# Kernel tuning notes

Measured on AMD Instinct MI355X. Metric: run time of the kernel, lower is better.

The kernel has to match this reference:

```python
import jax, jax.numpy as jnp
import numpy as np

D = 768

def setup_inputs() -> dict:
    key = jax.random.key(0)
    ks = jax.random.split(key, 12)
    inp = {
        "text_embeddings": jax.random.normal(ks[0], (8, 512, D), dtype=jnp.float32),
        "kb_emb": jax.random.normal(ks[1], (200000, D), dtype=jnp.float32),
        "W_ret": jax.random.normal(ks[2], (D, D), dtype=jnp.float32) * 0.02,
        "b_ret": jax.random.normal(ks[3], (D,), dtype=jnp.float32) * 0.02,
        "Ws1": jax.random.normal(ks[4], (2 * D, D), dtype=jnp.float32) * 0.02,
        "bs1": jax.random.normal(ks[5], (D,), dtype=jnp.float32) * 0.02,
        "Ws2": jax.random.normal(ks[6], (D, 1), dtype=jnp.float32) * 0.02,
        "bs2": jax.random.normal(ks[7], (1,), dtype=jnp.float32) * 0.02,
        "mention_sent": jax.random.randint(ks[8], (256,), 0, 8, dtype=jnp.int32),
        "mention_start": jax.random.randint(ks[9], (256,), 0, 480, dtype=jnp.int32),
        "mention_len": jax.random.randint(ks[10], (256,), 0, 31, dtype=jnp.int32),
        "top_k": 100,
    }
    return inp


def reference(text_embeddings, kb_emb, W_ret, b_ret, Ws1, bs1, Ws2, bs2,
              mention_sent, mention_start, mention_len, top_k):
    S = text_embeddings.shape[1]
    pos = jnp.arange(S, dtype=jnp.int32)
    # inclusive span [start, start+len] -> mask [M, S]
    mask = (pos[None, :] >= mention_start[:, None]) & (pos[None, :] <= (mention_start + mention_len)[:, None])
    maskf = mask.astype(text_embeddings.dtype)
    sent = text_embeddings[mention_sent]                       # [M, S, D]
    mention_emb = jnp.einsum('msd,ms->md', sent, maskf) / maskf.sum(1, keepdims=True)

    # entity_retriever linear, then KB dot-product retrieval of top 2k candidates
    query = mention_emb @ W_ret.T + b_ret                      # [M, D]
    sims = query @ kb_emb.T                                    # [M, N]
    _, cand_idx = jax.lax.top_k(sims, 2 * top_k)               # [M, 2k]
    cand_embs = kb_emb[cand_idx]                               # [M, 2k, D]

    # candidate_scorer: Linear(2D->D) on concat(mention, cand) + ReLU + Linear(D->1) + Sigmoid
    m_part = mention_emb @ Ws1[:D]                             # [M, D]
    c_part = jnp.einsum('mkd,de->mke', cand_embs, Ws1[D:])     # [M, 2k, D]
    h = jax.nn.relu(m_part[:, None, :] + c_part + bs1)
    scores = jax.nn.sigmoid(jnp.einsum('mke,eo->mko', h, Ws2)[..., 0] + bs2[0])  # [M, 2k]

    top_scores, ti = jax.lax.top_k(scores, top_k)              # [M, k]
    top_kb_idx = jnp.take_along_axis(cand_idx, ti, axis=1)
    return top_scores, top_kb_idx
```

## Files before the change

kernel.cpp:

```cpp
#include <hip/hip_runtime.h>
#include <cfloat>
#include <cmath>
#include <cstdint>

#define DD 768
#define MM 256
#define NKB 200000
#define SLEN 512
#define KK 200
#define TOPK 100
#define SURV_CAP 1024
#define RESC 232
#define THRC 2.70f
#define MAXMARK 32768
#define DELTA 4e-5
#define NET 12

typedef __attribute__((ext_vector_type(8))) short bf16x8;
typedef __attribute__((ext_vector_type(4))) float f32x4;

__device__ __forceinline__ unsigned short f2bf_rne(float x) {
  unsigned u = __float_as_uint(x);
  unsigned r = (u + 0x7FFFu + ((u >> 16) & 1u)) >> 16;
  return (unsigned short)r;
}
__device__ __forceinline__ float bf2f(unsigned short us) {
  return __uint_as_float(((unsigned)us) << 16);
}
__device__ __forceinline__ void splitbf(float x, unsigned short& hi, unsigned short& lo) {
  hi = f2bf_rne(x);
  lo = f2bf_rne(x - bf2f(hi));
}

__global__ __launch_bounds__(256) void k_mention_emb(
    const float* __restrict__ text, const int* __restrict__ msent,
    const int* __restrict__ mstart, const int* __restrict__ mlen,
    double* __restrict__ me64) {
  int m = blockIdx.x;
  int sent = msent[m], st = mstart[m], ln = mlen[m];
  const float* base = text + (size_t)sent * SLEN * DD;
  for (int d = threadIdx.x; d < DD; d += blockDim.x) {
    double acc = 0.0;
    for (int s = st; s <= st + ln; ++s) acc += (double)base[(size_t)s * DD + d];
    me64[(size_t)m * DD + d] = acc / (double)(ln + 1);
  }
}

__global__ __launch_bounds__(256) void k_query(
    const double* __restrict__ me64, const float* __restrict__ Wret,
    const float* __restrict__ bret, double* __restrict__ q64,
    unsigned short* __restrict__ qb16, float* __restrict__ tthr) {
  int m = blockIdx.x;
  __shared__ double sme[DD];
  __shared__ float snorm[256];
  for (int d = threadIdx.x; d < DD; d += blockDim.x) sme[d] = me64[(size_t)m * DD + d];
  __syncthreads();
  float nloc = 0.f;
  for (int e = threadIdx.x; e < DD; e += blockDim.x) {
    double acc = (double)bret[e];
    const float* wr = Wret + (size_t)e * DD;
    for (int d = 0; d < DD; ++d) acc += sme[d] * (double)wr[d];
    q64[(size_t)m * DD + e] = acc;
    qb16[(size_t)m * DD + e] = f2bf_rne((float)acc);
    nloc += (float)(acc * acc);
  }
  snorm[threadIdx.x] = nloc; __syncthreads();
  for (int s = 128; s > 0; s >>= 1) {
    if (threadIdx.x < s) snorm[threadIdx.x] += snorm[threadIdx.x + s];
    __syncthreads();
  }
  if (threadIdx.x == 0) tthr[m] = THRC * sqrtf(snorm[0]);
}

__global__ __launch_bounds__(256) void k_mpart(
    const double* __restrict__ me64, const float* __restrict__ Ws1,
    double* __restrict__ mp64, float* __restrict__ mp32) {
  int m = blockIdx.x;
  __shared__ double sme[DD];
  for (int d = threadIdx.x; d < DD; d += blockDim.x) sme[d] = me64[(size_t)m * DD + d];
  __syncthreads();
  for (int e = threadIdx.x; e < DD; e += blockDim.x) {
    double acc = 0.0;
    for (int d = 0; d < DD; ++d) acc += sme[d] * (double)Ws1[(size_t)d * DD + e];
    mp64[(size_t)m * DD + e] = acc;
    mp32[(size_t)m * DD + e] = (float)acc;
  }
}

__global__ __launch_bounds__(256) void k_prep(
    const float* __restrict__ Ws1, unsigned short* __restrict__ Bth,
    unsigned short* __restrict__ Btl) {
  int e = blockIdx.x;
  for (int k = threadIdx.x; k < DD; k += 256) {
    float x = Ws1[(size_t)(DD + k) * DD + e];
    unsigned short hi, lo;
    splitbf(x, hi, lo);
    Bth[(size_t)e * DD + k] = hi;
    Btl[(size_t)e * DD + k] = lo;
  }
}

__global__ __launch_bounds__(256) void k_sims_mfma(
    const unsigned short* __restrict__ qb, const float* __restrict__ kb,
    const float* __restrict__ tthr, int* __restrict__ gcnt,
    uint2* __restrict__ gcand) {
  __shared__ unsigned short As[256 * 32];
  __shared__ unsigned short Bs[64 * 32];
  __shared__ float sthr[256];
  int n0 = blockIdx.x * 64;
  int tid = threadIdx.x;
  int lane = tid & 63, w = tid >> 6;
  int h = lane >> 4, c = lane & 15;
  sthr[tid] = tthr[tid];
  f32x4 acc[4][4] = {};
  for (int k0 = 0; k0 < DD; k0 += 32) {
#pragma unroll
    for (int i = 0; i < 4; ++i) {
      int idx = tid + i * 256;
      int m = idx >> 2, q4 = idx & 3;
      uint4 v = *(const uint4*)(qb + (size_t)m * DD + k0 + q4 * 8);
      int off = (m * 64 + q4 * 16) ^ ((m & 7) << 4);
      *(uint4*)((char*)As + off) = v;
    }
#pragma unroll
    for (int i = 0; i < 2; ++i) {
      int idx = tid + i * 256;
      int n = idx >> 3, f4 = idx & 7;
      float4 v = *(const float4*)(kb + (size_t)(n0 + n) * DD + k0 + f4 * 4);
      uint2 p;
      p.x = (unsigned)f2bf_rne(v.x) | ((unsigned)f2bf_rne(v.y) << 16);
      p.y = (unsigned)f2bf_rne(v.z) | ((unsigned)f2bf_rne(v.w) << 16);
      int off = (n * 64 + f4 * 8) ^ ((n & 7) << 4);
      *(uint2*)((char*)Bs + off) = p;
    }
    __syncthreads();
    bf16x8 a[4], b[4];
#pragma unroll
    for (int mf = 0; mf < 4; ++mf) {
      int m = w * 64 + mf * 16 + c;
      int off = (m * 64 + h * 16) ^ ((m & 7) << 4);
      a[mf] = *(bf16x8*)((char*)As + off);
    }
#pragma unroll
    for (int nf = 0; nf < 4; ++nf) {
      int n = nf * 16 + c;
      int off = (n * 64 + h * 16) ^ ((n & 7) << 4);
      b[nf] = *(bf16x8*)((char*)Bs + off);
    }
#pragma unroll
    for (int mf = 0; mf < 4; ++mf)
#pragma unroll
      for (int nf = 0; nf < 4; ++nf)
        acc[mf][nf] = __builtin_amdgcn_mfma_f32_16x16x32_bf16(a[mf], b[nf], acc[mf][nf], 0, 0, 0);
    __syncthreads();
  }
#pragma unroll
  for (int mf = 0; mf < 4; ++mf)
#pragma unroll
    for (int nf = 0; nf < 4; ++nf)
#pragma unroll
      for (int r = 0; r < 4; ++r) {
        int row = w * 64 + mf * 16 + h * 4 + r;
        int col = n0 + nf * 16 + c;
        float v = acc[mf][nf][r];
        if (v > sthr[row]) {
          int p = atomicAdd(&gcnt[row], 1);
          if (p < SURV_CAP) gcand[(size_t)row * SURV_CAP + p] = make_uint2(__float_as_uint(v), (unsigned)col);
        }
      }
}

__global__ __launch_bounds__(256) void k_select(
    const uint2* __restrict__ gcand, const int* __restrict__ gcnt,
    const float* __restrict__ kb, const double* __restrict__ q64,
    int* __restrict__ cidx) {
  int m = blockIdx.x;
  __shared__ float skf[SURV_CAP];
  __shared__ int   sidx[SURV_CAP];
  __shared__ double sq[DD];
  __shared__ double skey[256];
  __shared__ int    skidx[256];
  int tid = threadIdx.x;
  int cnt = gcnt[m]; if (cnt > SURV_CAP) cnt = SURV_CAP;
  for (int d = tid; d < DD; d += 256) sq[d] = q64[(size_t)m * DD + d];
  for (int i = tid; i < SURV_CAP; i += 256) {
    if (i < cnt) {
      uint2 v = gcand[(size_t)m * SURV_CAP + i];
      skf[i] = __uint_as_float(v.x);
      sidx[i] = (int)v.y;
    } else { skf[i] = -FLT_MAX; sidx[i] = 0x7fffffff; }
  }
  __syncthreads();
  for (int k = 2; k <= SURV_CAP; k <<= 1) {
    for (int j = k >> 1; j > 0; j >>= 1) {
      for (int i = tid; i < SURV_CAP; i += 256) {
        int l = i ^ j;
        if (l > i) {
          float ka = skf[i], kb2 = skf[l];
          int ia = sidx[i], ib = sidx[l];
          bool lBefore = (kb2 > ka) || (kb2 == ka && ib < ia);
          bool iBefore = (ka > kb2) || (ka == kb2 && ia < ib);
          bool dir = ((i & k) == 0);
          bool sw = dir ? lBefore : iBefore;
          if (sw) { skf[i] = kb2; skf[l] = ka; sidx[i] = ib; sidx[l] = ia; }
        }
      }
      __syncthreads();
    }
  }
  int lane = tid & 63, wv = tid >> 6;
  for (int cpos = wv; cpos < RESC; cpos += 4) {
    int ci = sidx[cpos];
    double s;
    if (ci < NKB) {
      const float* krow = kb + (size_t)ci * DD;
      double acc = 0.0;
      for (int d = lane; d < DD; d += 64) acc += sq[d] * (double)krow[d];
      for (int off2 = 32; off2 > 0; off2 >>= 1) acc += __shfl_down(acc, off2, 64);
      s = acc;
    } else s = -INFINITY;
    if (lane == 0) { skey[cpos] = s; skidx[cpos] = ci; }
  }
  if (tid >= RESC && tid < 256) { skey[tid] = -INFINITY; skidx[tid] = 0x7fffffff; }
  __syncthreads();
  for (int k = 2; k <= 256; k <<= 1) {
    for (int j = k >> 1; j > 0; j >>= 1) {
      int i = tid, l = i ^ j;
      if (l > i) {
        double ka = skey[i], kb2 = skey[l];
        int ia = skidx[i], ib = skidx[l];
        bool lBefore = (kb2 > ka) || (kb2 == ka && ib < ia);
        bool iBefore = (ka > kb2) || (ka == kb2 && ia < ib);
        bool dir = ((i & k) == 0);
        bool sw = dir ? lBefore : iBefore;
        if (sw) { skey[i] = kb2; skey[l] = ka; skidx[i] = ib; skidx[l] = ia; }
      }
      __syncthreads();
    }
  }
  for (int cc = tid; cc < KK; cc += 256) {
    int v = skidx[cc];
    cidx[(size_t)m * KK + cc] = (v < NKB) ? v : 0;
  }
}

__global__ __launch_bounds__(256) void k_score2(
    const float* __restrict__ kb, const int* __restrict__ cidx,
    const float* __restrict__ mp32, const unsigned short* __restrict__ Bth,
    const unsigned short* __restrict__ Btl, const float* __restrict__ bs1,
    const float* __restrict__ Ws2, float* __restrict__ gpart) {
  __shared__ unsigned short Ah[256 * 32], Al[256 * 32];
  __shared__ unsigned short Bh[64 * 32], Bl[64 * 32];
  __shared__ float smp[3][64], sb1v[64], sw2v[64];
  __shared__ int srow[256];
  int p = blockIdx.x;
  int x = p & 7, j = p >> 3;
  int ct = x + 8 * (j / NET), et = j % NET;
  int r0 = ct * 256, e0 = et * 64;
  int tid = threadIdx.x, lane = tid & 63, w = tid >> 6;
  int h = lane >> 4, c = lane & 15;
  srow[tid] = cidx[r0 + tid];
  int m0 = r0 / KK;
  int mm1 = (m0 + 1 < MM) ? m0 + 1 : MM - 1;
  int mm2 = (m0 + 2 < MM) ? m0 + 2 : MM - 1;
  if (tid < 64) {
    smp[0][tid] = mp32[(size_t)m0 * DD + e0 + tid];
    smp[1][tid] = mp32[(size_t)mm1 * DD + e0 + tid];
    smp[2][tid] = mp32[(size_t)mm2 * DD + e0 + tid];
    sb1v[tid] = bs1[e0 + tid];
    sw2v[tid] = Ws2[e0 + tid];
  }
  __syncthreads();
  f32x4 acc[4][4] = {};
  for (int k0 = 0; k0 < DD; k0 += 32) {
#pragma unroll
    for (int it = 0; it < 8; ++it) {
      int idx = tid + it * 256;
      int rr = idx >> 3, f4 = idx & 7;
      float4 v = *(const float4*)(kb + (size_t)srow[rr] * DD + k0 + f4 * 4);
      unsigned short h0, h1, h2, h3, l0, l1, l2, l3;
      splitbf(v.x, h0, l0); splitbf(v.y, h1, l1);
      splitbf(v.z, h2, l2); splitbf(v.w, h3, l3);
      uint2 ph, pl;
      ph.x = (unsigned)h0 | ((unsigned)h1 << 16); ph.y = (unsigned)h2 | ((unsigned)h3 << 16);
      pl.x = (unsigned)l0 | ((unsigned)l1 << 16); pl.y = (unsigned)l2 | ((unsigned)l3 << 16);
      int off = (rr * 64 + f4 * 8) ^ ((rr & 7) << 4);
      *(uint2*)((char*)Ah + off) = ph;
      *(uint2*)((char*)Al + off) = pl;
    }
    {
      int e = tid >> 2, k8 = tid & 3;
      uint4 vh = *(const uint4*)(Bth + (size_t)(e0 + e) * DD + k0 + k8 * 8);
      uint4 vl = *(const uint4*)(Btl + (size_t)(e0 + e) * DD + k0 + k8 * 8);
      int off = (e * 64 + k8 * 16) ^ ((e & 7) << 4);
      *(uint4*)((char*)Bh + off) = vh;
      *(uint4*)((char*)Bl + off) = vl;
    }
    __syncthreads();
    bf16x8 ah[4], al[4];
#pragma unroll
    for (int mf = 0; mf < 4; ++mf) {
      int rr = w * 64 + mf * 16 + c;
      int off = (rr * 64 + h * 16) ^ ((rr & 7) << 4);
      ah[mf] = *(bf16x8*)((char*)Ah + off);
      al[mf] = *(bf16x8*)((char*)Al + off);
    }
#pragma unroll
    for (int nf = 0; nf < 4; ++nf) {
      int e = nf * 16 + c;
      int off = (e * 64 + h * 16) ^ ((e & 7) << 4);
      bf16x8 bh = *(bf16x8*)((char*)Bh + off);
      bf16x8 bl = *(bf16x8*)((char*)Bl + off);
#pragma unroll
      for (int mf = 0; mf < 4; ++mf) {
        acc[mf][nf] = __builtin_amdgcn_mfma_f32_16x16x32_bf16(ah[mf], bh, acc[mf][nf], 0, 0, 0);
        acc[mf][nf] = __builtin_amdgcn_mfma_f32_16x16x32_bf16(ah[mf], bl, acc[mf][nf], 0, 0, 0);
        acc[mf][nf] = __builtin_amdgcn_mfma_f32_16x16x32_bf16(al[mf], bh, acc[mf][nf], 0, 0, 0);
      }
    }
    __syncthreads();
  }
  int bnd1 = (m0 + 1) * KK, bnd2 = (m0 + 2) * KK;
#pragma unroll
  for (int mf = 0; mf < 4; ++mf) {
    float zp[4] = {0.f, 0.f, 0.f, 0.f};
#pragma unroll
    for (int nf = 0; nf < 4; ++nf) {
      int el = nf * 16 + c;
      float b1v = sb1v[el], w2v = sw2v[el];
#pragma unroll
      for (int r = 0; r < 4; ++r) {
        int rowg = r0 + w * 64 + mf * 16 + h * 4 + r;
        int sel = (rowg >= bnd1) + (rowg >= bnd2);
        float hh = acc[mf][nf][r] + smp[sel][el] + b1v;
        if (hh > 0.f) zp[r] += hh * w2v;
      }
    }
#pragma unroll
    for (int r = 0; r < 4; ++r) {
      float v = zp[r];
      v += __shfl_xor(v, 1, 64);
      v += __shfl_xor(v, 2, 64);
      v += __shfl_xor(v, 4, 64);
      v += __shfl_xor(v, 8, 64);
      if (c == 0)
        gpart[(size_t)(r0 + w * 64 + mf * 16 + h * 4 + r) * NET + et] = v;
    }
  }
}

__global__ __launch_bounds__(256) void k_zred(
    const float* __restrict__ gpart, const float* __restrict__ bs2,
    double* __restrict__ z64) {
  int r = blockIdx.x * 256 + threadIdx.x;
  double s = 0.0;
#pragma unroll
  for (int i = 0; i < NET; ++i) s += (double)gpart[(size_t)r * NET + i];
  z64[r] = s + (double)bs2[0];
}

__global__ __launch_bounds__(256) void k_mark(
    const double* __restrict__ z64, int* __restrict__ marks, int* __restrict__ mcnt) {
  int m = blockIdx.x;
  __shared__ double sk[256];
  __shared__ int sp[256];
  __shared__ int flag[256];
  int tid = threadIdx.x;
  flag[tid] = 0;
  if (tid < KK) { sk[tid] = z64[(size_t)m * KK + tid]; sp[tid] = tid; }
  else { sk[tid] = -INFINITY; sp[tid] = 0x7fffffff; }
  __syncthreads();
  for (int k = 2; k <= 256; k <<= 1) {
    for (int j = k >> 1; j > 0; j >>= 1) {
      int i = tid, l = i ^ j;
      if (l > i) {
        double ka = sk[i], kb2 = sk[l];
        int ia = sp[i], ib = sp[l];
        bool lBefore = (kb2 > ka) || (kb2 == ka && ib < ia);
        bool iBefore = (ka > kb2) || (ka == kb2 && ia < ib);
        bool dir = ((i & k) == 0);
        bool sw = dir ? lBefore : iBefore;
        if (sw) { sk[i] = kb2; sk[l] = ka; sp[i] = ib; sp[l] = ia; }
      }
      __syncthreads();
    }
  }
  if (tid <= 120) {
    if (sk[tid] - sk[tid + 1] < DELTA) {
      flag[tid] = 1;
      atomicExch(&flag[tid + 1], 1);
    }
  }
  __syncthreads();
  if (tid <= 121 && flag[tid]) {
    int p = atomicAdd(mcnt, 1);
    if (p < MAXMARK) marks[p] = m * KK + sp[tid];
  }
}

__global__ __launch_bounds__(256) void k_rescore(
    const float* __restrict__ kb, const int* __restrict__ cidx,
    const double* __restrict__ mp64, const float* __restrict__ Ws1,
    const float* __restrict__ bs1, const float* __restrict__ Ws2,
    const float* __restrict__ bs2, const int* __restrict__ marks,
    const int* __restrict__ mcnt, double* __restrict__ z64) {
  int cnt = *mcnt; if (cnt > MAXMARK) cnt = MAXMARK;
  __shared__ float sc[DD];
  __shared__ double sred[256];
  int tid = threadIdx.x;
  for (int it = blockIdx.x; it < cnt; it += gridDim.x) {
    int r = marks[it];
    int m = r / KK;
    int row = cidx[r];
    for (int d = tid; d < DD; d += 256) sc[d] = kb[(size_t)row * DD + d];
    __syncthreads();
    double pz = 0.0;
    for (int e = tid; e < DD; e += 256) {
      double a = 0.0;
      for (int d = 0; d < DD; ++d) a += (double)sc[d] * (double)Ws1[(size_t)(DD + d) * DD + e];
      double hv = mp64[(size_t)m * DD + e] + a + (double)bs1[e];
      if (hv > 0) pz += hv * (double)Ws2[e];
    }
    sred[tid] = pz; __syncthreads();
    for (int s = 128; s > 0; s >>= 1) { if (tid < s) sred[tid] += sred[tid + s]; __syncthreads(); }
    if (tid == 0) z64[r] = sred[0] + (double)bs2[0];
    __syncthreads();
  }
}

__global__ __launch_bounds__(256) void k_final(
    const double* __restrict__ z64, const int* __restrict__ cidx, float* __restrict__ out) {
  int m = blockIdx.x;
  __shared__ double sk[256];
  __shared__ int sp[256];
  int tid = threadIdx.x;
  if (tid < KK) { sk[tid] = z64[(size_t)m * KK + tid]; sp[tid] = tid; }
  else { sk[tid] = -INFINITY; sp[tid] = 0x7fffffff; }
  __syncthreads();
  for (int k = 2; k <= 256; k <<= 1) {
    for (int j = k >> 1; j > 0; j >>= 1) {
      int i = tid, l = i ^ j;
      if (l > i) {
        double ka = sk[i], kb2 = sk[l];
        int ia = sp[i], ib = sp[l];
        bool lBefore = (kb2 > ka) || (kb2 == ka && ib < ia);
        bool iBefore = (ka > kb2) || (ka == kb2 && ia < ib);
        bool dir = ((i & k) == 0);
        bool sw = dir ? lBefore : iBefore;
        if (sw) { sk[i] = kb2; sk[l] = ka; sp[i] = ib; sp[l] = ia; }
      }
      __syncthreads();
    }
  }
  if (tid < TOPK) {
    double z = sk[tid];
    out[(size_t)m * TOPK + tid] = (float)(1.0 / (1.0 + exp(-z)));
    out[(size_t)MM * TOPK + (size_t)m * TOPK + tid] = (float)cidx[(size_t)m * KK + sp[tid]];
  }
}

extern "C" void kernel_launch(void* const* d_in, const int* in_sizes, int n_in,
                              void* d_out, int out_size, void* d_ws, size_t ws_size,
                              hipStream_t stream) {
  const float* text  = (const float*)d_in[0];
  const float* kb    = (const float*)d_in[1];
  const float* Wret  = (const float*)d_in[2];
  const float* bret  = (const float*)d_in[3];
  const float* Ws1   = (const float*)d_in[4];
  const float* bs1   = (const float*)d_in[5];
  const float* Ws2   = (const float*)d_in[6];
  const float* bs2   = (const float*)d_in[7];
  const int* msent   = (const int*)d_in[8];
  const int* mstart  = (const int*)d_in[9];
  const int* mlen    = (const int*)d_in[10];
  float* out = (float*)d_out;

  char* ws = (char*)d_ws;
  size_t off = 0;
  auto alloc = [&](size_t bytes) -> void* {
    void* p = ws + off;
    off = (off + bytes + 255) & ~(size_t)255;
    return p;
  };
  double* me64 = (double*)alloc((size_t)MM * DD * 8);
  double* q64  = (double*)alloc((size_t)MM * DD * 8);
  unsigned short* qb16 = (unsigned short*)alloc((size_t)MM * DD * 2);
  float*  tthr = (float*) alloc((size_t)MM * 4);
  double* mp64 = (double*)alloc((size_t)MM * DD * 8);
  float*  mp32 = (float*) alloc((size_t)MM * DD * 4);
  int*    cidx = (int*)   alloc((size_t)MM * KK * 4);
  double* z64  = (double*)alloc((size_t)MM * KK * 8);
  float*  gpart = (float*)alloc((size_t)MM * KK * NET * 4);
  int*    marks = (int*)  alloc((size_t)MAXMARK * 4);
  int*    mcnt  = (int*)  alloc(256);
  int*    gcnt  = (int*)  alloc((size_t)MM * 4);
  uint2*  gcand = (uint2*)alloc((size_t)MM * SURV_CAP * 8);
  unsigned short* Bth = (unsigned short*)alloc((size_t)DD * DD * 2);
  unsigned short* Btl = (unsigned short*)alloc((size_t)DD * DD * 2);
  (void)ws_size;

  k_mention_emb<<<MM, 256, 0, stream>>>(text, msent, mstart, mlen, me64);
  k_query<<<MM, 256, 0, stream>>>(me64, Wret, bret, q64, qb16, tthr);
  k_mpart<<<MM, 256, 0, stream>>>(me64, Ws1, mp64, mp32);
  k_prep<<<DD, 256, 0, stream>>>(Ws1, Bth, Btl);

  hipMemsetAsync(gcnt, 0, (size_t)MM * 4, stream);
  k_sims_mfma<<<NKB / 64, 256, 0, stream>>>(qb16, kb, tthr, gcnt, gcand);
  k_select<<<MM, 256, 0, stream>>>(gcand, gcnt, kb, q64, cidx);

  k_score2<<<(MM * KK / 256) * NET, 256, 0, stream>>>(kb, cidx, mp32, Bth, Btl, bs1, Ws2, gpart);
  k_zred<<<MM * KK / 256, 256, 0, stream>>>(gpart, bs2, z64);
  hipMemsetAsync(mcnt, 0, 4, stream);
  k_mark<<<MM, 256, 0, stream>>>(z64, marks, mcnt);
  k_rescore<<<2048, 256, 0, stream>>>(kb, cidx, mp64, Ws1, bs1, Ws2, bs2, marks, mcnt, z64);
  k_final<<<MM, 256, 0, stream>>>(z64, cidx, out);
}
```

Baseline: 1.424 ms.

## Restructure KB similarity GEMM: 512 threads, direct A loads, prefetched B

The similarity kernel now runs 512 threads per block, and each wave owns 32 query rows instead of 64. The query tile is no longer staged through shared memory; each wave reads its A fragments straight from global memory, which should mostly hit in cache. The next 32-wide slice of KB rows is loaded into registers while the current slice is converted and stored, so the global loads overlap the MFMA work. The goal is to cut LDS traffic and occupancy pressure and to hide KB streaming latency, at the cost of more global A loads and two barriers per step.

```diff
diff --git a/kernel.cpp b/kernel.cpp
--- a/kernel.cpp
+++ b/kernel.cpp
@@ -100,67 +100,62 @@
   }
 }
 
-__global__ __launch_bounds__(256) void k_sims_mfma(
+__global__ __launch_bounds__(512) void k_sims_mfma(
     const unsigned short* __restrict__ qb, const float* __restrict__ kb,
     const float* __restrict__ tthr, int* __restrict__ gcnt,
     uint2* __restrict__ gcand) {
-  __shared__ unsigned short As[256 * 32];
   __shared__ unsigned short Bs[64 * 32];
   __shared__ float sthr[256];
   int n0 = blockIdx.x * 64;
   int tid = threadIdx.x;
   int lane = tid & 63, w = tid >> 6;
   int h = lane >> 4, c = lane & 15;
-  sthr[tid] = tthr[tid];
-  f32x4 acc[4][4] = {};
-  for (int k0 = 0; k0 < DD; k0 += 32) {
-#pragma unroll
-    for (int i = 0; i < 4; ++i) {
-      int idx = tid + i * 256;
-      int m = idx >> 2, q4 = idx & 3;
-      uint4 v = *(const uint4*)(qb + (size_t)m * DD + k0 + q4 * 8);
-      int off = (m * 64 + q4 * 16) ^ ((m & 7) << 4);
-      *(uint4*)((char*)As + off) = v;
-    }
-#pragma unroll
-    for (int i = 0; i < 2; ++i) {
-      int idx = tid + i * 256;
-      int n = idx >> 3, f4 = idx & 7;
-      float4 v = *(const float4*)(kb + (size_t)(n0 + n) * DD + k0 + f4 * 4);
-      uint2 p;
-      p.x = (unsigned)f2bf_rne(v.x) | ((unsigned)f2bf_rne(v.y) << 16);
-      p.y = (unsigned)f2bf_rne(v.z) | ((unsigned)f2bf_rne(v.w) << 16);
-      int off = (n * 64 + f4 * 8) ^ ((n & 7) << 4);
-      *(uint2*)((char*)Bs + off) = p;
-    }
-    __syncthreads();
-    bf16x8 a[4], b[4];
-#pragma unroll
-    for (int mf = 0; mf < 4; ++mf) {
-      int m = w * 64 + mf * 16 + c;
-      int off = (m * 64 + h * 16) ^ ((m & 7) << 4);
-      a[mf] = *(bf16x8*)((char*)As + off);
-    }
+  if (tid < 256) sthr[tid] = tthr[tid];
+  f32x4 acc[2][4] = {};
+  const int brow = n0 + (tid >> 3);
+  const int bk4  = (tid & 7) * 4;
+  const int bwoff = ((tid >> 3) * 64 + (tid & 7) * 8) ^ (((tid >> 3) & 7) << 4);
+  auto ldB = [&](int k0, float4 &dst) {
+    dst = *(const float4*)(kb + (size_t)brow * DD + k0 + bk4);
+  };
+  auto stB = [&](const float4 &v) {
+    uint2 p;
+    p.x = (unsigned)f2bf_rne(v.x) | ((unsigned)f2bf_rne(v.y) << 16);
+    p.y = (unsigned)f2bf_rne(v.z) | ((unsigned)f2bf_rne(v.w) << 16);
+    *(uint2*)((char*)Bs + bwoff) = p;
+  };
+  const unsigned short* qa0 = qb + (size_t)(w * 32 + c) * DD;
+  const unsigned short* qa1 = qb + (size_t)(w * 32 + 16 + c) * DD;
+  auto step = [&](int k0, float4 &cur, float4 &nxt, bool pf) {
+    bf16x8 a0 = *(const bf16x8*)(qa0 + k0 + h * 8);
+    bf16x8 a1 = *(const bf16x8*)(qa1 + k0 + h * 8);
+    __syncthreads();
+    stB(cur);
+    if (pf) ldB(k0 + 32, nxt);
+    __syncthreads();
 #pragma unroll
     for (int nf = 0; nf < 4; ++nf) {
       int n = nf * 16 + c;
       int off = (n * 64 + h * 16) ^ ((n & 7) << 4);
-      b[nf] = *(bf16x8*)((char*)Bs + off);
-    }
-#pragma unroll
-    for (int mf = 0; mf < 4; ++mf)
-#pragma unroll
-      for (int nf = 0; nf < 4; ++nf)
-        acc[mf][nf] = __builtin_amdgcn_mfma_f32_16x16x32_bf16(a[mf], b[nf], acc[mf][nf], 0, 0, 0);
-    __syncthreads();
-  }
-#pragma unroll
-  for (int mf = 0; mf < 4; ++mf)
+      bf16x8 b = *(bf16x8*)((char*)Bs + off);
+      acc[0][nf] = __builtin_amdgcn_mfma_f32_16x16x32_bf16(a0, b, acc[0][nf], 0, 0, 0);
+      acc[1][nf] = __builtin_amdgcn_mfma_f32_16x16x32_bf16(a1, b, acc[1][nf], 0, 0, 0);
+    }
+  };
+  float4 b0, b1;
+  ldB(0, b0);
+#pragma unroll
+  for (int kc = 0; kc < 12; ++kc) {
+    step(kc * 64,      b0, b1, true);
+    step(kc * 64 + 32, b1, b0, kc < 11);
+  }
+#pragma unroll
+  for (int mf = 0; mf < 2; ++mf)
 #pragma unroll
     for (int nf = 0; nf < 4; ++nf)
 #pragma unroll
       for (int r = 0; r < 4; ++r) {
-        int row = w * 64 + mf * 16 + h * 4 + r;
+        int row = w * 32 + mf * 16 + h * 4 + r;
         int col = n0 + nf * 16 + c;
         float v = acc[mf][nf][r];
         if (v > sthr[row]) {
@@ -505,7 +500,7 @@
   k_prep<<<DD, 256, 0, stream>>>(Ws1, Bth, Btl);
 
   hipMemsetAsync(gcnt, 0, (size_t)MM * 4, stream);
-  k_sims_mfma<<<NKB / 64, 256, 0, stream>>>(qb16, kb, tthr, gcnt, gcand);
+  k_sims_mfma<<<NKB / 64, 512, 0, stream>>>(qb16, kb, tthr, gcnt, gcand);
   k_select<<<MM, 256, 0, stream>>>(gcand, gcnt, kb, q64, cidx);
 
   k_score2<<<(MM * KK / 256) * NET, 256, 0, stream>>>(kb, cidx, mp32, Bth, Btl, bs1, Ws2, gpart);
```

Measured after the change: 1.341 ms. 5.8% less time.
